# Kernel tuning notes

Measured on AMD Instinct MI355X. Metric: run time of the kernel, lower is better.

Reference implementation:

```python
import jax, jax.numpy as jnp
import numpy as np

N_NODES = 100000


def gcn_conv(x, src, dst, w, W, b, n):
    """PyG GCNConv: out = D^{-1/2} (A+I) D^{-1/2} (x @ W) + b (self-loops weight 1)."""
    loop = jnp.arange(n, dtype=src.dtype)
    s = jnp.concatenate([src, loop])
    d = jnp.concatenate([dst, loop])
    ew = jnp.concatenate([w, jnp.ones((n,), x.dtype)])
    deg = jax.ops.segment_sum(ew, d, num_segments=n)            # degree of target nodes
    dinv = jnp.where(deg > 0, jax.lax.rsqrt(deg), jnp.zeros_like(deg))
    norm = dinv[s] * ew * dinv[d]                               # [E+N]
    h = x @ W                                                   # [N, out] dense transform first
    msg = h[s] * norm[:, None]                                  # gather + scale
    out = jax.ops.segment_sum(msg, d, num_segments=n)           # scatter-add aggregate
    return out + b


def setup_inputs() -> dict:
    key = jax.random.key(0)
    k1, k2, k3, k4, k5, k6 = jax.random.split(key, 6)
    in_dim, hid, out_dim = 128, 128, 64
    n_edges = 1600000
    x = jax.random.normal(k1, (N_NODES, in_dim), dtype=jnp.float32)
    edge_index = jax.random.randint(k2, (2, n_edges), 0, N_NODES, dtype=jnp.int32)
    edge_weight = jax.random.uniform(k3, (n_edges,), dtype=jnp.float32)
    # Glorot-style weights, zero bias (as in GCNConv defaults)
    W1 = jax.random.normal(k4, (in_dim, hid), dtype=jnp.float32) / np.sqrt(in_dim)
    b1 = jnp.zeros((hid,), jnp.float32)
    W2 = jax.random.normal(k5, (hid, out_dim), dtype=jnp.float32) / np.sqrt(hid)
    b2 = jnp.zeros((out_dim,), jnp.float32)
    return {"x": x, "edge_index": edge_index, "edge_weight": edge_weight,
            "W1": W1, "b1": b1, "W2": W2, "b2": b2}


def reference(x, edge_index, edge_weight, W1, b1, W2, b2):
    src, dst = edge_index[0], edge_index[1]
    h = gcn_conv(x, src, dst, edge_weight, W1, b1, N_NODES)
    h = jax.nn.relu(h)
    # dropout is identity in eval mode
    out = gcn_conv(h, src, dst, edge_weight, W2, b2, N_NODES)
    return out
```

## Files before the change

kernel.cpp:

```cpp
#include <hip/hip_runtime.h>
#include <cstdint>
#include <cstddef>


typedef unsigned long long u64;
typedef unsigned int u32;
typedef unsigned short u16;

__device__ __forceinline__ float bflo(u32 u) { return __uint_as_float(u << 16); }
__device__ __forceinline__ float bfhi(u32 u) { return __uint_as_float(u & 0xffff0000u); }
__device__ __forceinline__ u32 f2bf(float f) {
  u32 u = __float_as_uint(f);
  return (u + 0x7fffu + ((u >> 16) & 1u)) >> 16;
}
__device__ __forceinline__ u32 pack2bf(float lo, float hi) {
  return f2bf(lo) | (f2bf(hi) << 16);
}

__global__ void init_kernel(u64* packed, int n) {
  int i = blockIdx.x * 256 + threadIdx.x;
  if (i < n) packed[i] = (1ull << 32);
}

__global__ __launch_bounds__(256) void fused_dg_kernel(
    const int* __restrict__ dst, const float* __restrict__ ew,
    u64* packed, u16* __restrict__ rank, int E, int degBlocks,
    const float* __restrict__ x, const float* __restrict__ W1,
    u16* __restrict__ h1, int M) {
  if ((int)blockIdx.x < degBlocks) {
    int e = blockIdx.x * 256 + threadIdx.x;
    if (e < E) {
      int d = dst[e];
      u64 add = (1ull << 48) | (u64)((double)ew[e] * 4294967296.0);
      u64 old = atomicAdd(&packed[d], add);
      rank[e] = (u16)(old >> 48);
    }
    return;
  }
  __shared__ float As[128][64];
  __shared__ float Ws[128][64];
  const int gb = blockIdx.x - degBlocks;
  const int nbx = (M + 63) >> 6;
  const int bx = gb % nbx;
  const int by = gb / nbx;
  const int tid = threadIdx.x;
  const int tx = tid & 15;
  const int ty = tid >> 4;
  const int rowbase = bx * 64;
  const int colbase = by * 64;

  for (int i = tid; i < 64 * 32; i += 256) {
    int row = i & 63;
    int k4 = (i >> 6) << 2;
    int gr = rowbase + row;
    float4 v = make_float4(0.f, 0.f, 0.f, 0.f);
    if (gr < M) v = *reinterpret_cast<const float4*>(x + (size_t)gr * 128 + k4);
    As[k4 + 0][row] = v.x;
    As[k4 + 1][row] = v.y;
    As[k4 + 2][row] = v.z;
    As[k4 + 3][row] = v.w;
  }
  for (int i = tid; i < 128 * 16; i += 256) {
    int c4 = (i & 15) << 2;
    int k = i >> 4;
    float4 v = *reinterpret_cast<const float4*>(W1 + (size_t)k * 128 + colbase + c4);
    *reinterpret_cast<float4*>(&Ws[k][c4]) = v;
  }
  __syncthreads();

  float acc[4][4] = {};
  #pragma unroll 8
  for (int k = 0; k < 128; ++k) {
    float4 a = *reinterpret_cast<const float4*>(&As[k][ty << 2]);
    float4 b = *reinterpret_cast<const float4*>(&Ws[k][tx << 2]);
    acc[0][0] += a.x * b.x; acc[0][1] += a.x * b.y; acc[0][2] += a.x * b.z; acc[0][3] += a.x * b.w;
    acc[1][0] += a.y * b.x; acc[1][1] += a.y * b.y; acc[1][2] += a.y * b.z; acc[1][3] += a.y * b.w;
    acc[2][0] += a.z * b.x; acc[2][1] += a.z * b.y; acc[2][2] += a.z * b.z; acc[2][3] += a.z * b.w;
    acc[3][0] += a.w * b.x; acc[3][1] += a.w * b.y; acc[3][2] += a.w * b.z; acc[3][3] += a.w * b.w;
  }
  #pragma unroll
  for (int r = 0; r < 4; ++r) {
    int gr = rowbase + (ty << 2) + r;
    if (gr < M) {
      uint2 p;
      p.x = pack2bf(acc[r][0], acc[r][1]);
      p.y = pack2bf(acc[r][2], acc[r][3]);
      *reinterpret_cast<uint2*>(h1 + (size_t)gr * 128 + colbase + (tx << 2)) = p;
    }
  }
}

__global__ void scan1_kernel(const u64* __restrict__ packed, int* __restrict__ rowstart,
                             int* __restrict__ bsum, float* __restrict__ dinvp, int n) {
  __shared__ int wsum[4];
  int b = blockIdx.x;
  int base = b * 1024;
  int tid = threadIdx.x;
  int lane = tid & 63, wv = tid >> 6;
  int idx = base + tid * 4;
  int v0 = 0, v1 = 0, v2 = 0, v3 = 0;
  #pragma unroll
  for (int j = 0; j < 4; ++j) {
    if (idx + j < n) {
      u64 p = packed[idx + j];
      int c = (int)(p >> 48);
      if (j == 0) v0 = c; else if (j == 1) v1 = c; else if (j == 2) v2 = c; else v3 = c;
      float deg = (float)((double)(p & 0xFFFFFFFFFFFFull) * 2.3283064365386963e-10);
      dinvp[idx + j] = rsqrtf(deg);
    }
  }
  int tsum = v0 + v1 + v2 + v3;
  int inc = tsum;
  #pragma unroll
  for (int off = 1; off < 64; off <<= 1) {
    int u = __shfl_up(inc, off, 64);
    if (lane >= off) inc += u;
  }
  if (lane == 63) wsum[wv] = inc;
  __syncthreads();
  int woff = 0;
  for (int w2 = 0; w2 < wv; ++w2) woff += wsum[w2];
  int texc = woff + inc - tsum;
  if (idx     < n) rowstart[idx]     = texc;
  if (idx + 1 < n) rowstart[idx + 1] = texc + v0;
  if (idx + 2 < n) rowstart[idx + 2] = texc + v0 + v1;
  if (idx + 3 < n) rowstart[idx + 3] = texc + v0 + v1 + v2;
  if (tid == 255) bsum[b] = woff + inc;
}

__global__ void scan2_kernel(const int* __restrict__ bsum, int* __restrict__ boff, int nblk) {
  __shared__ int wsum[4];
  int tid = threadIdx.x, lane = tid & 63, wv = tid >> 6;
  int v = (tid < nblk) ? bsum[tid] : 0;
  int inc = v;
  #pragma unroll
  for (int off = 1; off < 64; off <<= 1) {
    int u = __shfl_up(inc, off, 64);
    if (lane >= off) inc += u;
  }
  if (lane == 63) wsum[wv] = inc;
  __syncthreads();
  int woff = 0;
  for (int w2 = 0; w2 < wv; ++w2) woff += wsum[w2];
  if (tid < nblk) boff[tid] = woff + inc - v;
}

__global__ void scan3_kernel(int* __restrict__ rowstart, const int* __restrict__ boff,
                             int n, int E) {
  int b = blockIdx.x;
  int base = b * 1024;
  int off = boff[b];
  for (int j = threadIdx.x; j < 1024; j += 256) {
    int i = base + j;
    if (i < n) rowstart[i] += off;
  }
  if (b == 0 && threadIdx.x == 0) rowstart[n] = E;
}

__global__ void fill_kernel(const int* __restrict__ src, const int* __restrict__ dst,
                            const float* __restrict__ w, const u16* __restrict__ rank,
                            const float* __restrict__ dinv, const int* __restrict__ rowstart,
                            int2* __restrict__ erec, int E) {
  int e = blockIdx.x * 256 + threadIdx.x;
  if (e < E) {
    int s = src[e], d = dst[e];
    int pos = rowstart[d] + (int)rank[e];
    float nrm = dinv[s] * w[e] * dinv[d];
    erec[pos] = make_int2(s, __float_as_int(nrm));
  }
}

__global__ __launch_bounds__(256) void gemm2_kernel(const u16* __restrict__ A,
                                                    const float* __restrict__ W,
                                                    u16* __restrict__ C, int M) {
  __shared__ float As[128][64];
  __shared__ float Ws[128][64];
  const int tid = threadIdx.x;
  const int tx = tid & 15;
  const int ty = tid >> 4;
  const int rowbase = blockIdx.x * 64;

  for (int i = tid; i < 64 * 32; i += 256) {
    int row = i & 63;
    int chunk = i >> 6;
    int k4 = chunk << 2;
    int gr = rowbase + row;
    float f0 = 0.f, f1 = 0.f, f2 = 0.f, f3 = 0.f;
    if (gr < M) {
      uint2 u = reinterpret_cast<const uint2*>(A + (size_t)gr * 128)[chunk];
      f0 = bflo(u.x); f1 = bfhi(u.x); f2 = bflo(u.y); f3 = bfhi(u.y);
    }
    As[k4 + 0][row] = f0;
    As[k4 + 1][row] = f1;
    As[k4 + 2][row] = f2;
    As[k4 + 3][row] = f3;
  }
  for (int i = tid; i < 128 * 16; i += 256) {
    int c4 = (i & 15) << 2;
    int k = i >> 4;
    float4 v = *reinterpret_cast<const float4*>(W + (size_t)k * 64 + c4);
    *reinterpret_cast<float4*>(&Ws[k][c4]) = v;
  }
  __syncthreads();

  float acc[4][4] = {};
  #pragma unroll 8
  for (int k = 0; k < 128; ++k) {
    float4 a = *reinterpret_cast<const float4*>(&As[k][ty << 2]);
    float4 b = *reinterpret_cast<const float4*>(&Ws[k][tx << 2]);
    acc[0][0] += a.x * b.x; acc[0][1] += a.x * b.y; acc[0][2] += a.x * b.z; acc[0][3] += a.x * b.w;
    acc[1][0] += a.y * b.x; acc[1][1] += a.y * b.y; acc[1][2] += a.y * b.z; acc[1][3] += a.y * b.w;
    acc[2][0] += a.z * b.x; acc[2][1] += a.z * b.y; acc[2][2] += a.z * b.z; acc[2][3] += a.z * b.w;
    acc[3][0] += a.w * b.x; acc[3][1] += a.w * b.y; acc[3][2] += a.w * b.z; acc[3][3] += a.w * b.w;
  }
  #pragma unroll
  for (int r = 0; r < 4; ++r) {
    int gr = rowbase + (ty << 2) + r;
    if (gr < M) {
      uint2 p;
      p.x = pack2bf(acc[r][0], acc[r][1]);
      p.y = pack2bf(acc[r][2], acc[r][3]);
      *reinterpret_cast<uint2*>(C + (size_t)gr * 64 + (tx << 2)) = p;
    }
  }
}

__global__ __launch_bounds__(256) void agg128_relu_kernel(
    const u32* __restrict__ H, const int* __restrict__ rowstart,
    const int2* __restrict__ erec, const float* __restrict__ dinv,
    const float* __restrict__ bias, u32* __restrict__ out, int n) {
  int wid = (blockIdx.x * 256 + threadIdx.x) >> 6;
  int lane = threadIdx.x & 63;
  if (wid >= n) return;
  float dv = dinv[wid];
  float ns = dv * dv;
  u32 hv = H[(size_t)wid * 64 + lane];
  float a0 = ns * bflo(hv), a1 = ns * bfhi(hv);
  int e0 = rowstart[wid], e1 = rowstart[wid + 1];
  int e = e0;
  for (; e + 3 < e1; e += 4) {
    int2 r0 = erec[e], r1 = erec[e + 1], r2 = erec[e + 2], r3 = erec[e + 3];
    u32 v0 = H[(size_t)r0.x * 64 + lane];
    u32 v1 = H[(size_t)r1.x * 64 + lane];
    u32 v2 = H[(size_t)r2.x * 64 + lane];
    u32 v3 = H[(size_t)r3.x * 64 + lane];
    float w0 = __int_as_float(r0.y), w1 = __int_as_float(r1.y);
    float w2 = __int_as_float(r2.y), w3 = __int_as_float(r3.y);
    a0 += w0 * bflo(v0) + w1 * bflo(v1) + w2 * bflo(v2) + w3 * bflo(v3);
    a1 += w0 * bfhi(v0) + w1 * bfhi(v1) + w2 * bfhi(v2) + w3 * bfhi(v3);
  }
  for (; e < e1; ++e) {
    int2 r = erec[e];
    u32 v = H[(size_t)r.x * 64 + lane];
    float w = __int_as_float(r.y);
    a0 += w * bflo(v);
    a1 += w * bfhi(v);
  }
  float2 bb = reinterpret_cast<const float2*>(bias)[lane];
  a0 = fmaxf(a0 + bb.x, 0.f);
  a1 = fmaxf(a1 + bb.y, 0.f);
  out[(size_t)wid * 64 + lane] = pack2bf(a0, a1);
}

__global__ __launch_bounds__(256) void agg64_kernel(
    const u16* __restrict__ H, const int* __restrict__ rowstart,
    const int2* __restrict__ erec, const float* __restrict__ dinv,
    const float* __restrict__ bias, float* __restrict__ out, int n) {
  int wid = (blockIdx.x * 256 + threadIdx.x) >> 6;
  int lane = threadIdx.x & 63;
  if (wid >= n) return;
  float dv = dinv[wid];
  float ns = dv * dv;
  float a0 = ns * bflo((u32)H[(size_t)wid * 64 + lane]);
  int e0 = rowstart[wid], e1 = rowstart[wid + 1];
  int e = e0;
  for (; e + 3 < e1; e += 4) {
    int2 r0 = erec[e], r1 = erec[e + 1], r2 = erec[e + 2], r3 = erec[e + 3];
    float v0 = bflo((u32)H[(size_t)r0.x * 64 + lane]);
    float v1 = bflo((u32)H[(size_t)r1.x * 64 + lane]);
    float v2 = bflo((u32)H[(size_t)r2.x * 64 + lane]);
    float v3 = bflo((u32)H[(size_t)r3.x * 64 + lane]);
    a0 += __int_as_float(r0.y) * v0 + __int_as_float(r1.y) * v1 +
          __int_as_float(r2.y) * v2 + __int_as_float(r3.y) * v3;
  }
  for (; e < e1; ++e) {
    int2 r = erec[e];
    a0 += __int_as_float(r.y) * bflo((u32)H[(size_t)r.x * 64 + lane]);
  }
  out[(size_t)wid * 64 + lane] = a0 + bias[lane];
}

extern "C" void kernel_launch(void* const* d_in, const int* in_sizes, int n_in,
                              void* d_out, int out_size, void* d_ws, size_t ws_size,
                              hipStream_t stream) {
  const float* x  = (const float*)d_in[0];
  const int*   ei = (const int*)d_in[1];
  const float* ew = (const float*)d_in[2];
  const float* W1 = (const float*)d_in[3];
  const float* b1 = (const float*)d_in[4];
  const float* W2 = (const float*)d_in[5];
  const float* b2 = (const float*)d_in[6];
  float* out = (float*)d_out;
  const int N = in_sizes[0] / 128;
  const int E = in_sizes[2];
  const int* src = ei;
  const int* dst = ei + E;

  char* wsB = (char*)d_ws;
  size_t off = 0;
  auto alloc = [&](size_t bytes) {
    void* p = wsB + off;
    off += ((bytes + 255) / 256) * 256;
    return p;
  };
  u64*   packed = (u64*)alloc((size_t)N * 8);
  float* dinv   = (float*)alloc((size_t)N * 4);
  u16*   rank   = (u16*)alloc((size_t)E * 2);
  int*   rowst  = (int*)alloc((size_t)(N + 1) * 4);
  int*   bsum   = (int*)alloc(256 * 4);
  int*   boff   = (int*)alloc(256 * 4);
  int2*  erec   = (int2*)alloc((size_t)E * 8);
  u16*   h1     = (u16*)alloc((size_t)N * 128 * 2);
  u16*   a1     = (u16*)alloc((size_t)N * 128 * 2);
  u16*   h2     = h1;

  const int nb = (N + 255) / 256;
  const int eb = (E + 255) / 256;
  const int nbx = (N + 63) / 64;
  const int gemm1Blocks = nbx * 2;
  const int nblk = (N + 1023) / 1024;

  init_kernel<<<nb, 256, 0, stream>>>(packed, N);
  fused_dg_kernel<<<eb + gemm1Blocks, 256, 0, stream>>>(
      dst, ew, packed, rank, E, eb, x, W1, h1, N);
  scan1_kernel<<<nblk, 256, 0, stream>>>(packed, rowst, bsum, dinv, N);
  scan2_kernel<<<1, 256, 0, stream>>>(bsum, boff, nblk);
  scan3_kernel<<<nblk, 256, 0, stream>>>(rowst, boff, N, E);
  fill_kernel<<<eb, 256, 0, stream>>>(src, dst, ew, rank, dinv, rowst, erec, E);

  const int ab = (N + 3) / 4;
  agg128_relu_kernel<<<ab, 256, 0, stream>>>((const u32*)h1, rowst, erec, dinv, b1,
                                             (u32*)a1, N);
  gemm2_kernel<<<nbx, 256, 0, stream>>>(a1, W2, h2, N);
  agg64_kernel<<<ab, 256, 0, stream>>>(h2, rowst, erec, dinv, b2, out, N);
}
```

Measured before the change: 461.9 us.

## Drop scan3 pass by folding block offsets into consumers; split degree/GEMM1 kernel

Removes the third scan kernel that added per-block offsets to the row pointers. Instead fill and both aggregation kernels add boff[row>>10] when they read rowstart, and scan1 writes the local end value for rowstart[n]. The fused degree-atomic/GEMM1 kernel is split into two separate launches, and the fixed-point weight conversion now uses float instead of double. This saves a launch and a pass over rowstart, but loses the overlap between the atomics and the GEMM and adds a small extra load in the consumers.

```diff
diff --git a/kernel.cpp b/kernel.cpp
--- a/kernel.cpp
+++ b/kernel.cpp
@@ -22,32 +22,27 @@
   if (i < n) packed[i] = (1ull << 32);
 }
 
-__global__ __launch_bounds__(256) void fused_dg_kernel(
-    const int* __restrict__ dst, const float* __restrict__ ew,
-    u64* packed, u16* __restrict__ rank, int E, int degBlocks,
-    const float* __restrict__ x, const float* __restrict__ W1,
-    u16* __restrict__ h1, int M) {
-  if ((int)blockIdx.x < degBlocks) {
-    int e = blockIdx.x * 256 + threadIdx.x;
-    if (e < E) {
-      int d = dst[e];
-      u64 add = (1ull << 48) | (u64)((double)ew[e] * 4294967296.0);
-      u64 old = atomicAdd(&packed[d], add);
-      rank[e] = (u16)(old >> 48);
-    }
-    return;
-  }
+__global__ void degrank_kernel(const int* __restrict__ dst, const float* __restrict__ w,
+                               u64* packed, u16* __restrict__ rank, int E) {
+  int e = blockIdx.x * 256 + threadIdx.x;
+  if (e < E) {
+    int d = dst[e];
+    u64 add = (1ull << 48) | (u64)(w[e] * 4294967296.0f);
+    u64 old = atomicAdd(&packed[d], add);
+    rank[e] = (u16)(old >> 48);
+  }
+}
+
+__global__ __launch_bounds__(256) void gemm1_kernel(const float* __restrict__ x,
+                                                    const float* __restrict__ W1,
+                                                    u16* __restrict__ h1, int M) {
   __shared__ float As[128][64];
   __shared__ float Ws[128][64];
-  const int gb = blockIdx.x - degBlocks;
-  const int nbx = (M + 63) >> 6;
-  const int bx = gb % nbx;
-  const int by = gb / nbx;
   const int tid = threadIdx.x;
   const int tx = tid & 15;
   const int ty = tid >> 4;
-  const int rowbase = bx * 64;
-  const int colbase = by * 64;
+  const int rowbase = blockIdx.x * 64;
+  const int colbase = blockIdx.y * 64;
 
   for (int i = tid; i < 64 * 32; i += 256) {
     int row = i & 63;
@@ -125,7 +120,10 @@
   if (idx + 1 < n) rowstart[idx + 1] = texc + v0;
   if (idx + 2 < n) rowstart[idx + 2] = texc + v0 + v1;
   if (idx + 3 < n) rowstart[idx + 3] = texc + v0 + v1 + v2;
-  if (tid == 255) bsum[b] = woff + inc;
+  if (tid == 255) {
+    bsum[b] = woff + inc;
+    if (b == (int)gridDim.x - 1) rowstart[n] = woff + inc;
+  }
 }
 
 __global__ void scan2_kernel(const int* __restrict__ bsum, int* __restrict__ boff, int nblk) {
@@ -145,26 +143,14 @@
   if (tid < nblk) boff[tid] = woff + inc - v;
 }
 
-__global__ void scan3_kernel(int* __restrict__ rowstart, const int* __restrict__ boff,
-                             int n, int E) {
-  int b = blockIdx.x;
-  int base = b * 1024;
-  int off = boff[b];
-  for (int j = threadIdx.x; j < 1024; j += 256) {
-    int i = base + j;
-    if (i < n) rowstart[i] += off;
-  }
-  if (b == 0 && threadIdx.x == 0) rowstart[n] = E;
-}
-
 __global__ void fill_kernel(const int* __restrict__ src, const int* __restrict__ dst,
                             const float* __restrict__ w, const u16* __restrict__ rank,
                             const float* __restrict__ dinv, const int* __restrict__ rowstart,
-                            int2* __restrict__ erec, int E) {
+                            const int* __restrict__ boff, int2* __restrict__ erec, int E) {
   int e = blockIdx.x * 256 + threadIdx.x;
   if (e < E) {
     int s = src[e], d = dst[e];
-    int pos = rowstart[d] + (int)rank[e];
+    int pos = rowstart[d] + boff[d >> 10] + (int)rank[e];
     float nrm = dinv[s] * w[e] * dinv[d];
     erec[pos] = make_int2(s, __float_as_int(nrm));
   }
@@ -227,8 +213,9 @@
 
 __global__ __launch_bounds__(256) void agg128_relu_kernel(
     const u32* __restrict__ H, const int* __restrict__ rowstart,
-    const int2* __restrict__ erec, const float* __restrict__ dinv,
-    const float* __restrict__ bias, u32* __restrict__ out, int n) {
+    const int* __restrict__ boff, const int2* __restrict__ erec,
+    const float* __restrict__ dinv, const float* __restrict__ bias,
+    u32* __restrict__ out, int n) {
   int wid = (blockIdx.x * 256 + threadIdx.x) >> 6;
   int lane = threadIdx.x & 63;
   if (wid >= n) return;
@@ -236,7 +223,8 @@
   float ns = dv * dv;
   u32 hv = H[(size_t)wid * 64 + lane];
   float a0 = ns * bflo(hv), a1 = ns * bfhi(hv);
-  int e0 = rowstart[wid], e1 = rowstart[wid + 1];
+  int e0 = rowstart[wid] + boff[wid >> 10];
+  int e1 = rowstart[wid + 1] + boff[(wid + 1) >> 10];
   int e = e0;
   for (; e + 3 < e1; e += 4) {
     int2 r0 = erec[e], r1 = erec[e + 1], r2 = erec[e + 2], r3 = erec[e + 3];
@@ -264,15 +252,17 @@
 
 __global__ __launch_bounds__(256) void agg64_kernel(
     const u16* __restrict__ H, const int* __restrict__ rowstart,
-    const int2* __restrict__ erec, const float* __restrict__ dinv,
-    const float* __restrict__ bias, float* __restrict__ out, int n) {
+    const int* __restrict__ boff, const int2* __restrict__ erec,
+    const float* __restrict__ dinv, const float* __restrict__ bias,
+    float* __restrict__ out, int n) {
   int wid = (blockIdx.x * 256 + threadIdx.x) >> 6;
   int lane = threadIdx.x & 63;
   if (wid >= n) return;
   float dv = dinv[wid];
   float ns = dv * dv;
   float a0 = ns * bflo((u32)H[(size_t)wid * 64 + lane]);
-  int e0 = rowstart[wid], e1 = rowstart[wid + 1];
+  int e0 = rowstart[wid] + boff[wid >> 10];
+  int e1 = rowstart[wid + 1] + boff[(wid + 1) >> 10];
   int e = e0;
   for (; e + 3 < e1; e += 4) {
     int2 r0 = erec[e], r1 = erec[e + 1], r2 = erec[e + 2], r3 = erec[e + 3];
@@ -327,20 +317,19 @@
   const int nb = (N + 255) / 256;
   const int eb = (E + 255) / 256;
   const int nbx = (N + 63) / 64;
-  const int gemm1Blocks = nbx * 2;
   const int nblk = (N + 1023) / 1024;
 
   init_kernel<<<nb, 256, 0, stream>>>(packed, N);
-  fused_dg_kernel<<<eb + gemm1Blocks, 256, 0, stream>>>(
-      dst, ew, packed, rank, E, eb, x, W1, h1, N);
+  degrank_kernel<<<eb, 256, 0, stream>>>(dst, ew, packed, rank, E);
+  dim3 g1(nbx, 2);
+  gemm1_kernel<<<g1, 256, 0, stream>>>(x, W1, h1, N);
   scan1_kernel<<<nblk, 256, 0, stream>>>(packed, rowst, bsum, dinv, N);
   scan2_kernel<<<1, 256, 0, stream>>>(bsum, boff, nblk);
-  scan3_kernel<<<nblk, 256, 0, stream>>>(rowst, boff, N, E);
-  fill_kernel<<<eb, 256, 0, stream>>>(src, dst, ew, rank, dinv, rowst, erec, E);
+  fill_kernel<<<eb, 256, 0, stream>>>(src, dst, ew, rank, dinv, rowst, boff, erec, E);
 
   const int ab = (N + 3) / 4;
-  agg128_relu_kernel<<<ab, 256, 0, stream>>>((const u32*)h1, rowst, erec, dinv, b1,
+  agg128_relu_kernel<<<ab, 256, 0, stream>>>((const u32*)h1, rowst, boff, erec, dinv, b1,
                                              (u32*)a1, N);
   gemm2_kernel<<<nbx, 256, 0, stream>>>(a1, W2, h2, N);
-  agg64_kernel<<<ab, 256, 0, stream>>>(h2, rowst, erec, dinv, b2, out, N);
-}
+  agg64_kernel<<<ab, 256, 0, stream>>>(h2, rowst, boff, erec, dinv, b2, out, N);
+}
```

Result: slower. 472.7 us (+2.3%).
